# Optimization experiments

Measured on AMD Instinct MI355X. Metric: run time of the kernel, lower is better.

## Reference

```python
import jax, jax.numpy as jnp
import numpy as np

B, T, D = 64, 256, 300
H = 256            # each_state = state_size // 2
G = 4 * H          # gate dim = state_size * 2
N = 8              # num_bases
M, KQ = 64, 64     # meta_dim, key_query_size
V = 10000          # meta vocab


def setup_inputs() -> dict:
    key = jax.random.key(0)
    ks = jax.random.split(key, 16)
    s = 0.05
    return {
        'x': jax.random.normal(ks[0], (B, T, D), jnp.float32),
        'length': jax.random.randint(ks[1], (B,), 1, T + 1),
        'user_idx': jax.random.randint(ks[2], (B,), 0, V),
        'item_idx': jax.random.randint(ks[3], (B,), 0, V),
        'user_emb': jax.random.normal(ks[4], (V, M), jnp.float32) * s,
        'item_emb': jax.random.normal(ks[5], (V, M), jnp.float32) * s,
        'W1': jax.random.normal(ks[6], (2 * M, KQ), jnp.float32) * s,
        'b1': jax.random.normal(ks[7], (KQ,), jnp.float32) * s,
        'W2': jax.random.normal(ks[8], (KQ, N), jnp.float32) * s,
        'Wih': jax.random.normal(ks[9], (N, G, D), jnp.float32) * s,
        'Whh': jax.random.normal(ks[10], (N, G, H), jnp.float32) * s,
        'bias': jax.random.normal(ks[11], (N, G), jnp.float32) * s,
        'Wih_r': jax.random.normal(ks[12], (N, G, D), jnp.float32) * s,
        'Whh_r': jax.random.normal(ks[13], (N, G, H), jnp.float32) * s,
        'bias_r': jax.random.normal(ks[14], (N, G), jnp.float32) * s,
    }


def _run_dir(xs, mask, Wi, Wh, bb):
    # xs: [T,B,D], mask: [T,B] True where state forced to zero
    b, h = xs.shape[1], Wh.shape[2]
    h0 = jnp.zeros((b, h), xs.dtype)

    def step(carry, inp):
        hx, cx = carry
        xt, m = inp
        gates = (jnp.einsum('bgi,bi->bg', Wi, xt)
                 + jnp.einsum('bgh,bh->bg', Wh, hx) + bb)
        ig, fg, gg, og = jnp.split(gates, 4, axis=1)
        cy = jax.nn.sigmoid(fg) * cx + jax.nn.sigmoid(ig) * jnp.tanh(gg)
        hy = jax.nn.sigmoid(og) * jnp.tanh(cy)
        cy = jnp.where(m[:, None], 0.0, cy)
        hy = jnp.where(m[:, None], 0.0, hy)
        return (hy, cy), hy

    _, hs = jax.lax.scan(step, (h0, h0), (xs, mask))
    return hs  # [T,B,H]


def reference(x, length, user_idx, item_idx, user_emb, item_emb,
              W1, b1, W2, Wih, Whh, bias, Wih_r, Whh_r, bias_r):
    # basis mixing coefficients per sample
    q = jnp.concatenate([user_emb[user_idx], item_emb[item_idx]], axis=1)  # [B,2M]
    c = jax.nn.softmax(jnp.tanh(q @ W1 + b1) @ W2, axis=1)                 # [B,N]
    mix = lambda w: jnp.einsum('bn,n...->b...', c, w)

    Bc, Tc = x.shape[0], x.shape[1]
    t = jnp.arange(Tc)
    mask_f = t[:, None] >= length[None, :]            # length - 1 < i
    mask_r = (Tc - t)[:, None] > length[None, :]      # maxlength - i > length

    xs = jnp.swapaxes(x, 0, 1)                        # [T,B,D]
    h_f = _run_dir(xs, mask_f, mix(Wih), mix(Whh), mix(bias))
    h_r = _run_dir(xs[::-1], mask_r, mix(Wih_r), mix(Whh_r), mix(bias_r))
    h_r = h_r[::-1]                                   # un-reverse in time
    return jnp.concatenate([h_f, h_r], axis=-1).swapaxes(0, 1)  # [B,T,2H]
```

## Files before the change

### kernel.cpp

```cpp
#include <hip/hip_runtime.h>

#define B_ 64
#define T_ 256
#define D_ 300
#define DP_ 320
#define H_ 256
#define G_ 1024
#define N_ 8

typedef unsigned int u32;
typedef unsigned short u16;
typedef __attribute__((ext_vector_type(8))) short short8;
typedef __attribute__((ext_vector_type(4))) float f32x4;
typedef __attribute__((ext_vector_type(4))) u32 u32x4;
typedef __attribute__((ext_vector_type(2))) u32 u32x2;
typedef _Float16 h2 __attribute__((ext_vector_type(2)));
typedef __fp16 fp16x2 __attribute__((ext_vector_type(2)));

__device__ __forceinline__ u16 f2bf(float f){
  union {float f; u32 u;} v; v.f = f;
  u32 r = (v.u + 0x7fffu + ((v.u>>16)&1u)) >> 16;
  return (u16)r;
}
__device__ __forceinline__ float bflo(u32 u){
  union {u32 u; float f;} v; v.u = u<<16; return v.f;
}
__device__ __forceinline__ float bfhi(u32 u){
  union {u32 u; float f;} v; v.u = u & 0xffff0000u; return v.f;
}
__device__ __forceinline__ float sigm(float x){ return 1.0f/(1.0f+__expf(-x)); }
__device__ __forceinline__ float tanh_(float x){ return 2.0f/(1.0f+__expf(-2.0f*x)) - 1.0f; }

__device__ __forceinline__ float fdot2(u32 a, u32 b, float c){
  union { u32 u; h2 h; } ua, ub; ua.u = a; ub.u = b;
#if __has_builtin(__builtin_amdgcn_fdot2)
  return __builtin_amdgcn_fdot2(ua.h, ub.h, c, false);
#else
  return c + (float)ua.h.x*(float)ub.h.x + (float)ua.h.y*(float)ub.h.y;
#endif
}
__device__ __forceinline__ u32 pkf16(float a, float b){
  union { fp16x2 h; u32 u; } v; v.h = __builtin_amdgcn_cvt_pkrtz(a, b); return v.u;
}

__global__ void __launch_bounds__(64) k_coef(
    const int* __restrict__ uidx, const int* __restrict__ iidx,
    const float* __restrict__ uemb, const float* __restrict__ iemb,
    const float* __restrict__ W1, const float* __restrict__ b1,
    const float* __restrict__ W2, float* __restrict__ coef)
{
  __shared__ float q[128];
  __shared__ float hid[64];
  __shared__ float lg[8];
  int b = blockIdx.x, t = threadIdx.x;
  int u = uidx[b], it = iidx[b];
  q[t]      = uemb[(size_t)u*64 + t];
  q[64 + t] = iemb[(size_t)it*64 + t];
  __syncthreads();
  float s = b1[t];
  for (int j = 0; j < 128; ++j) s = fmaf(q[j], W1[j*64 + t], s);
  hid[t] = tanhf(s);
  __syncthreads();
  if (t < 8) {
    float s2 = 0.f;
    for (int j = 0; j < 64; ++j) s2 = fmaf(hid[j], W2[j*8 + t], s2);
    lg[t] = s2;
  }
  __syncthreads();
  if (t == 0) {
    float mx = lg[0];
    for (int n = 1; n < 8; ++n) mx = fmaxf(mx, lg[n]);
    float e[8], den = 0.f;
    for (int n = 0; n < 8; ++n){ e[n] = __expf(lg[n]-mx); den += e[n]; }
    for (int n = 0; n < 8; ++n) coef[b*8+n] = e[n]/den;
  }
}

__global__ void __launch_bounds__(256) k_mix_whh(
    const float* __restrict__ Whh_f, const float* __restrict__ Whh_r,
    const float* __restrict__ bias_f, const float* __restrict__ bias_r,
    const float* __restrict__ coef, u32* __restrict__ blob, float* __restrict__ bias_m)
{
  int gblk = blockIdx.x;
  int dir  = blockIdx.y;
  int tid  = threadIdx.x;
  const float* Wsel = dir ? Whh_r : Whh_f;
  const float* bsel = dir ? bias_r : bias_f;
  __shared__ float bs[N_][8][H_];
  for (int v = 0; v < 64; ++v){
    int i = v*256 + tid;
    int n = i >> 11, gl = (i >> 8) & 7, c = i & 255;
    bs[n][gl][c] = Wsel[((size_t)n*G_ + gblk*8 + gl)*H_ + c];
  }
  __syncthreads();
  int t2l = tid & 7, ii = tid >> 3;
  int tid2 = gblk*8 + t2l;
  int gg = tid2 >> 2, q = tid2 & 3;
  int cidx = ii >> 2, e = ii & 3;
  int p = q*32 + ((cidx + 2*q)&7)*4 + e;
  int glbase = gg*4 - gblk*8;
  float bw0[4][8], bw1[4][8];
  #pragma unroll
  for (int l = 0; l < 4; ++l)
    #pragma unroll
    for (int n = 0; n < 8; ++n){
      bw0[l][n] = bs[n][glbase + l][2*p];
      bw1[l][n] = bs[n][glbase + l][2*p + 1];
    }
  for (int b = 0; b < B_; ++b){
    float c8[8];
    #pragma unroll
    for (int n = 0; n < 8; ++n) c8[n] = coef[b*8+n];
    u32x4 ov;
    #pragma unroll
    for (int l = 0; l < 4; ++l){
      float w0 = 0.f, w1 = 0.f;
      #pragma unroll
      for (int n = 0; n < 8; ++n){ w0 = fmaf(c8[n], bw0[l][n], w0); w1 = fmaf(c8[n], bw1[l][n], w1); }
      ov[l] = pkf16(w0, w1);
    }
    size_t chain = (size_t)(dir*B_ + b);
    *(u32x4*)(blob + ((chain*32 + ii)*1024 + tid2)*4) = ov;
    if (tid < 8){
      float bb = 0.f;
      #pragma unroll
      for (int n = 0; n < 8; ++n) bb = fmaf(c8[n], bsel[n*G_ + gblk*8 + tid], bb);
      bias_m[chain*G_ + gblk*8 + tid] = bb;
    }
  }
}

__global__ void __launch_bounds__(256) k_mix_wi(
    const float* __restrict__ Wih_f, const float* __restrict__ Wih_r,
    const float* __restrict__ coef, u32* __restrict__ WimU)
{
  int gblk = blockIdx.x;
  int dir  = blockIdx.y;
  int tid  = threadIdx.x;
  const float* Wsel = dir ? Wih_r : Wih_f;
  __shared__ float bs[N_][8][D_];
  for (int v = 0; v < 75; ++v){
    int i = v*256 + tid;
    int n = i/2400, rem = i%2400, gl = rem/300, c = rem%300;
    bs[n][gl][c] = Wsel[((size_t)n*G_ + gblk*8 + gl)*D_ + c];
  }
  __syncthreads();
  float bw[5][2][8];
  int rowv[5], cpv[5];
  #pragma unroll
  for (int v = 0; v < 5; ++v){
    int idx = v*256 + tid;
    int row = idx/160, cp = idx%160;
    rowv[v] = row; cpv[v] = cp;
    #pragma unroll
    for (int n = 0; n < 8; ++n){
      bw[v][0][n] = (cp < 150) ? bs[n][row][2*cp]   : 0.f;
      bw[v][1][n] = (cp < 150) ? bs[n][row][2*cp+1] : 0.f;
    }
  }
  for (int b = 0; b < B_; ++b){
    float c8[8];
    #pragma unroll
    for (int n = 0; n < 8; ++n) c8[n] = coef[b*8+n];
    #pragma unroll
    for (int v = 0; v < 5; ++v){
      float w0 = 0.f, w1 = 0.f;
      #pragma unroll
      for (int n = 0; n < 8; ++n){ w0 = fmaf(c8[n], bw[v][0][n], w0); w1 = fmaf(c8[n], bw[v][1][n], w1); }
      WimU[(((size_t)(dir*B_+b)*G_ + gblk*8 + rowv[v])*160) + cpv[v]] = (u32)f2bf(w0) | ((u32)f2bf(w1) << 16);
    }
  }
}

__global__ void __launch_bounds__(256) k_xpad(const float* __restrict__ x, u32* __restrict__ xpadU)
{
  int o = blockIdx.x*256 + threadIdx.x;
  int bt = o/160, cp = o%160;
  float v0 = (cp < 150) ? x[(size_t)bt*D_ + 2*cp]   : 0.f;
  float v1 = (cp < 150) ? x[(size_t)bt*D_ + 2*cp+1] : 0.f;
  xpadU[o] = (u32)f2bf(v0) | ((u32)f2bf(v1) << 16);
}

__global__ void __launch_bounds__(256,2) k_gemm(
    const u16* __restrict__ xpad, const u16* __restrict__ Wim,
    const float* __restrict__ bias_m, u16* __restrict__ xproj)
{
  int bx = blockIdx.x;
  int b  = blockIdx.y, dir = blockIdx.z;
  int tt = bx >> 3, tg = bx & 7;
  int tid = threadIdx.x;
  int wid = tid >> 6, lane = tid & 63;
  int wr = wid >> 1, wc = wid & 1;
  __shared__ u16 As[128][72];
  __shared__ u16 Bs[128][72];
  const u16* Ap = xpad + ((size_t)b*T_ + tt*128)*DP_;
  const u16* Bp = Wim + (((size_t)dir*B_ + b)*G_ + tg*128)*DP_;
  f32x4 acc[4][4];
  #pragma unroll
  for (int i = 0; i < 4; ++i)
    #pragma unroll
    for (int j = 0; j < 4; ++j) acc[i][j] = (f32x4){0.f,0.f,0.f,0.f};
  for (int kt = 0; kt < 5; ++kt){
    int k0 = kt*64;
    #pragma unroll
    for (int i = 0; i < 4; ++i){
      int ci = i*256 + tid;
      int row = ci >> 3, cc = (ci & 7)*8;
      *(u32x4*)&As[row][cc] = *(const u32x4*)(Ap + (size_t)row*DP_ + k0 + cc);
      *(u32x4*)&Bs[row][cc] = *(const u32x4*)(Bp + (size_t)row*DP_ + k0 + cc);
    }
    __syncthreads();
    #pragma unroll
    for (int kk = 0; kk < 2; ++kk){
      short8 af[4], bfr[4];
      #pragma unroll
      for (int mi = 0; mi < 4; ++mi) af[mi]  = *(const short8*)&As[wr*64 + mi*16 + (lane&15)][kk*32 + (lane>>4)*8];
      #pragma unroll
      for (int ni = 0; ni < 4; ++ni) bfr[ni] = *(const short8*)&Bs[wc*64 + ni*16 + (lane&15)][kk*32 + (lane>>4)*8];
      #pragma unroll
      for (int mi = 0; mi < 4; ++mi)
        #pragma unroll
        for (int ni = 0; ni < 4; ++ni)
          acc[mi][ni] = __builtin_amdgcn_mfma_f32_16x16x32_bf16(af[mi], bfr[ni], acc[mi][ni], 0,0,0);
    }
    __syncthreads();
  }
  int r4 = (lane >> 4)*4, cg = lane & 15;
  const float* bmp = bias_m + (size_t)(dir*B_ + b)*G_;
  #pragma unroll
  for (int ni = 0; ni < 4; ++ni){
    int g = tg*128 + wc*64 + ni*16 + cg;
    float bsv = bmp[g];
    #pragma unroll
    for (int mi = 0; mi < 4; ++mi)
      #pragma unroll
      for (int j = 0; j < 4; ++j){
        int t = tt*128 + wr*64 + mi*16 + r4 + j;
        xproj[(((size_t)dir*B_ + b)*T_ + t)*G_ + g] = f2bf(acc[mi][ni][j] + bsv);
      }
  }
}

__global__ void __launch_bounds__(1024) k_rec(
    const u32* __restrict__ blob, const u32* __restrict__ xprojU,
    const int* __restrict__ length, float* __restrict__ out)
{
  int chain = blockIdx.x;
  int dir = chain >> 6, b = chain & 63;
  int tid = threadIdx.x;
  int gg = tid >> 2, q = tid & 3;
  __shared__ u32 wlds[8][1024][4];
  __shared__ __align__(16) float gates4[256][4];
  __shared__ __align__(16) u16 hp16[256];
  const u32* hp32 = (const u32*)hp16;

  u32 w[96];
  const u32* bp = blob + (size_t)chain*32*1024*4;
  #pragma unroll
  for (int ii = 0; ii < 24; ++ii){
    u32x4 v = *(const u32x4*)(bp + ((size_t)ii*1024 + tid)*4);
    w[4*ii] = v.x; w[4*ii+1] = v.y; w[4*ii+2] = v.z; w[4*ii+3] = v.w;
  }
  #pragma unroll
  for (int ii = 24; ii < 32; ++ii){
    u32x4 v = *(const u32x4*)(bp + ((size_t)ii*1024 + tid)*4);
    *(u32x4*)&wlds[ii-24][tid][0] = v;
  }
  if (tid < 256) hp16[tid] = 0;
  int len = length[b];
  const u32* xp = xprojU + (size_t)chain*T_*512;
  float* outp = out + (size_t)b*T_*512 + dir*H_;
  float cst = 0.f;
  __syncthreads();

  for (int step = 0; step < len; ++step){
    int t = dir ? (len-1-step) : step;
    u32 xv0 = 0, xv1 = 0;
    if (q == 0){
      u32x2 xv = *(const u32x2*)(xp + (size_t)t*512 + 2*gg);
      xv0 = xv.x; xv1 = xv.y;
    }
    float a0 = 0.f, a1 = 0.f, a2 = 0.f, a3 = 0.f;
    #pragma unroll
    for (int cidx = 0; cidx < 8; ++cidx){
      int c4 = (cidx + 2*q) & 7;
      u32x4 hq = *(const u32x4*)&hp32[q*32 + c4*4];
      if (cidx < 6){
        #pragma unroll
        for (int e = 0; e < 4; ++e){
          u32 hv = hq[e];
          a0 = fdot2(w[cidx*16 + e*4 + 0], hv, a0);
          a1 = fdot2(w[cidx*16 + e*4 + 1], hv, a1);
          a2 = fdot2(w[cidx*16 + e*4 + 2], hv, a2);
          a3 = fdot2(w[cidx*16 + e*4 + 3], hv, a3);
        }
      } else {
        #pragma unroll
        for (int e = 0; e < 4; ++e){
          u32x4 wv = *(const u32x4*)&wlds[cidx*4 + e - 24][tid][0];
          u32 hv = hq[e];
          a0 = fdot2(wv.x, hv, a0);
          a1 = fdot2(wv.y, hv, a1);
          a2 = fdot2(wv.z, hv, a2);
          a3 = fdot2(wv.w, hv, a3);
        }
      }
    }
    a0 += __shfl_xor(a0, 1); a0 += __shfl_xor(a0, 2);
    a1 += __shfl_xor(a1, 1); a1 += __shfl_xor(a1, 2);
    a2 += __shfl_xor(a2, 1); a2 += __shfl_xor(a2, 2);
    a3 += __shfl_xor(a3, 1); a3 += __shfl_xor(a3, 2);
    if (q == 0){
      a0 += bflo(xv0); a1 += bfhi(xv0); a2 += bflo(xv1); a3 += bfhi(xv1);
      f32x4 g4; g4.x = a0; g4.y = a1; g4.z = a2; g4.w = a3;
      *(f32x4*)&gates4[gg][0] = g4;
    }
    __syncthreads();
    if (tid < 256){
      const float* gf = &gates4[0][0];
      float ig = gf[tid],       fg = gf[256 + tid];
      float g_ = gf[512 + tid], og = gf[768 + tid];
      float i_ = sigm(ig), f_ = sigm(fg), gt = tanh_(g_), o_ = sigm(og);
      float cn = fmaf(f_, cst, i_*gt);
      float hy = o_ * tanh_(cn);
      cst = cn;
      ((u16*)hp16)[tid] = (u16)(pkf16(hy, hy) & 0xffffu);
      outp[(size_t)t*512 + tid] = hy;
    }
    __syncthreads();
  }
}

extern "C" void kernel_launch(void* const* d_in, const int* in_sizes, int n_in,
                              void* d_out, int out_size, void* d_ws, size_t ws_size,
                              hipStream_t stream)
{
  const float* x      = (const float*)d_in[0];
  const int*   length = (const int*)d_in[1];
  const int*   uidx   = (const int*)d_in[2];
  const int*   iidx   = (const int*)d_in[3];
  const float* uemb   = (const float*)d_in[4];
  const float* iemb   = (const float*)d_in[5];
  const float* W1     = (const float*)d_in[6];
  const float* b1     = (const float*)d_in[7];
  const float* W2     = (const float*)d_in[8];
  const float* Wih    = (const float*)d_in[9];
  const float* Whh    = (const float*)d_in[10];
  const float* bias   = (const float*)d_in[11];
  const float* Wih_r  = (const float*)d_in[12];
  const float* Whh_r  = (const float*)d_in[13];
  const float* bias_r = (const float*)d_in[14];
  float* out = (float*)d_out;
  char* ws = (char*)d_ws;

  float* coef   = (float*)(ws + 0);
  float* bias_m = (float*)(ws + 2048);
  u32*   blob   = (u32*)  (ws + 526336);
  u16*   Wim    = (u16*)  (ws + 67635200);
  u16*   xpad   = (u16*)  (ws + 151521280);
  u16*   xproj  = (u16*)  (ws + 162007040);

  (void)hipMemsetAsync(d_out, 0, (size_t)out_size*sizeof(float), stream);
  if (ws_size < 229115904ull) return;

  hipLaunchKernelGGL(k_coef,    dim3(64),       dim3(64),   0, stream, uidx, iidx, uemb, iemb, W1, b1, W2, coef);
  hipLaunchKernelGGL(k_mix_whh, dim3(128,2),    dim3(256),  0, stream, Whh, Whh_r, bias, bias_r, coef, blob, bias_m);
  hipLaunchKernelGGL(k_mix_wi,  dim3(128,2),    dim3(256),  0, stream, Wih, Wih_r, coef, (u32*)Wim);
  hipLaunchKernelGGL(k_xpad,    dim3(10240),    dim3(256),  0, stream, x, (u32*)xpad);
  hipLaunchKernelGGL(k_gemm,    dim3(16,64,2),  dim3(256),  0, stream, xpad, Wim, bias_m, xproj);
  hipLaunchKernelGGL(k_rec,     dim3(128),      dim3(1024), 0, stream, blob, (const u32*)xproj, length, out);
}
```

Measured before the change: 623.3 us.

## Keep all recurrent weights in registers, use DPP reductions and lighter barriers

The recurrent kernel now holds all 128 weight words per thread in registers instead of keeping a quarter of them in LDS, so the per-step LDS weight reads go away. The quad reduction switches from shfl_xor to DPP quad permutes. The __syncthreads calls become explicit lgkmcnt waits plus s_barrier, and the activations use a hardware reciprocal. With 1024 threads per block the register budget is tight (at most 128 VGPRs per thread at that size), so raising the array from 96 to 128 words risks spills to scratch.

Measured after the change: 1.154 ms. 1.85x slower.

```diff
diff --git a/kernel.cpp b/kernel.cpp
--- a/kernel.cpp
+++ b/kernel.cpp
@@ -28,8 +28,15 @@
 __device__ __forceinline__ float bfhi(u32 u){
   union {u32 u; float f;} v; v.u = u & 0xffff0000u; return v.f;
 }
-__device__ __forceinline__ float sigm(float x){ return 1.0f/(1.0f+__expf(-x)); }
-__device__ __forceinline__ float tanh_(float x){ return 2.0f/(1.0f+__expf(-2.0f*x)) - 1.0f; }
+__device__ __forceinline__ float rcp_(float x){
+#if __has_builtin(__builtin_amdgcn_rcpf)
+  return __builtin_amdgcn_rcpf(x);
+#else
+  return 1.0f/x;
+#endif
+}
+__device__ __forceinline__ float sigm(float x){ return rcp_(1.0f + __expf(-x)); }
+__device__ __forceinline__ float tanh_(float x){ return fmaf(2.0f, rcp_(1.0f + __expf(-2.0f*x)), -1.0f); }
 
 __device__ __forceinline__ float fdot2(u32 a, u32 b, float c){
   union { u32 u; h2 h; } ua, ub; ua.u = a; ub.u = b;
@@ -41,6 +48,14 @@
 }
 __device__ __forceinline__ u32 pkf16(float a, float b){
   union { fp16x2 h; u32 u; } v; v.h = __builtin_amdgcn_cvt_pkrtz(a, b); return v.u;
+}
+__device__ __forceinline__ float qred(float v){
+  union {float f; int i;} u, t;
+  u.f = v;
+  t.i = __builtin_amdgcn_mov_dpp(u.i, 0xB1, 0xF, 0xF, true);
+  u.f += t.f;
+  t.i = __builtin_amdgcn_mov_dpp(u.i, 0x4E, 0xF, 0xF, true);
+  return u.f + t.f;
 }
 
 __global__ void __launch_bounds__(64) k_coef(
@@ -249,22 +264,16 @@
   int dir = chain >> 6, b = chain & 63;
   int tid = threadIdx.x;
   int gg = tid >> 2, q = tid & 3;
-  __shared__ u32 wlds[8][1024][4];
   __shared__ __align__(16) float gates4[256][4];
   __shared__ __align__(16) u16 hp16[256];
   const u32* hp32 = (const u32*)hp16;
 
-  u32 w[96];
+  u32 w[128];
   const u32* bp = blob + (size_t)chain*32*1024*4;
   #pragma unroll
-  for (int ii = 0; ii < 24; ++ii){
+  for (int ii = 0; ii < 32; ++ii){
     u32x4 v = *(const u32x4*)(bp + ((size_t)ii*1024 + tid)*4);
     w[4*ii] = v.x; w[4*ii+1] = v.y; w[4*ii+2] = v.z; w[4*ii+3] = v.w;
-  }
-  #pragma unroll
-  for (int ii = 24; ii < 32; ++ii){
-    u32x4 v = *(const u32x4*)(bp + ((size_t)ii*1024 + tid)*4);
-    *(u32x4*)&wlds[ii-24][tid][0] = v;
   }
   if (tid < 256) hp16[tid] = 0;
   int len = length[b];
@@ -285,37 +294,24 @@
     for (int cidx = 0; cidx < 8; ++cidx){
       int c4 = (cidx + 2*q) & 7;
       u32x4 hq = *(const u32x4*)&hp32[q*32 + c4*4];
-      if (cidx < 6){
-        #pragma unroll
-        for (int e = 0; e < 4; ++e){
-          u32 hv = hq[e];
-          a0 = fdot2(w[cidx*16 + e*4 + 0], hv, a0);
-          a1 = fdot2(w[cidx*16 + e*4 + 1], hv, a1);
-          a2 = fdot2(w[cidx*16 + e*4 + 2], hv, a2);
-          a3 = fdot2(w[cidx*16 + e*4 + 3], hv, a3);
-        }
-      } else {
-        #pragma unroll
-        for (int e = 0; e < 4; ++e){
-          u32x4 wv = *(const u32x4*)&wlds[cidx*4 + e - 24][tid][0];
-          u32 hv = hq[e];
-          a0 = fdot2(wv.x, hv, a0);
-          a1 = fdot2(wv.y, hv, a1);
-          a2 = fdot2(wv.z, hv, a2);
-          a3 = fdot2(wv.w, hv, a3);
-        }
+      #pragma unroll
+      for (int e = 0; e < 4; ++e){
+        u32 hv = hq[e];
+        a0 = fdot2(w[cidx*16 + e*4 + 0], hv, a0);
+        a1 = fdot2(w[cidx*16 + e*4 + 1], hv, a1);
+        a2 = fdot2(w[cidx*16 + e*4 + 2], hv, a2);
+        a3 = fdot2(w[cidx*16 + e*4 + 3], hv, a3);
       }
     }
-    a0 += __shfl_xor(a0, 1); a0 += __shfl_xor(a0, 2);
-    a1 += __shfl_xor(a1, 1); a1 += __shfl_xor(a1, 2);
-    a2 += __shfl_xor(a2, 1); a2 += __shfl_xor(a2, 2);
-    a3 += __shfl_xor(a3, 1); a3 += __shfl_xor(a3, 2);
+    a0 = qred(a0); a1 = qred(a1); a2 = qred(a2); a3 = qred(a3);
     if (q == 0){
       a0 += bflo(xv0); a1 += bfhi(xv0); a2 += bflo(xv1); a3 += bfhi(xv1);
       f32x4 g4; g4.x = a0; g4.y = a1; g4.z = a2; g4.w = a3;
       *(f32x4*)&gates4[gg][0] = g4;
     }
-    __syncthreads();
+    asm volatile("s_waitcnt lgkmcnt(0)" ::: "memory");
+    __builtin_amdgcn_s_barrier();
+    __builtin_amdgcn_sched_barrier(0);
     if (tid < 256){
       const float* gf = &gates4[0][0];
       float ig = gf[tid],       fg = gf[256 + tid];
@@ -327,7 +323,9 @@
       ((u16*)hp16)[tid] = (u16)(pkf16(hy, hy) & 0xffffu);
       outp[(size_t)t*512 + tid] = hy;
     }
-    __syncthreads();
+    asm volatile("s_waitcnt lgkmcnt(0)" ::: "memory");
+    __builtin_amdgcn_s_barrier();
+    __builtin_amdgcn_sched_barrier(0);
   }
 }
 
```
